# Optimization experiments

Hardware: AMD Instinct MI355X
Metric: run time of the kernel (lower is better)

Reference implementation:

```python
import jax, jax.numpy as jnp
import numpy as np

B, N, DIM, H = 32, 3136, 768, 12
C = DIM // H  # head_dim = 64


def setup_inputs() -> dict:
    key = jax.random.key(0)
    k1, k2, k3, k4 = jax.random.split(key, 4)
    x = jax.random.normal(k1, (B, N, DIM), dtype=jnp.float32)
    # Linear weights stored as (in, out); qkv has no bias (qkv_bias=False)
    w_qkv = jax.random.normal(k2, (DIM, 3 * DIM), dtype=jnp.float32) * (1.0 / np.sqrt(DIM))
    w_proj = jax.random.normal(k3, (DIM, DIM), dtype=jnp.float32) * (1.0 / np.sqrt(DIM))
    b_proj = jax.random.normal(k4, (DIM,), dtype=jnp.float32) * 0.01
    return {"x": x, "w_qkv": w_qkv, "w_proj": w_proj, "b_proj": b_proj}


def reference(x, w_qkv, w_proj, b_proj):
    # qkv projection: [B,N,3*DIM] -> [3,B,H,N,C]
    qkv = (x @ w_qkv).reshape(B, N, 3, H, C).transpose(2, 0, 3, 1, 4)
    q, k, v = qkv[0], qkv[1], qkv[2]
    # Efficient (linear) attention: softmax q over channel dim, k over token dim
    q = jax.nn.softmax(q, axis=-1)                      # [B,H,N,C], softmax over C
    kt = jax.nn.softmax(k.transpose(0, 1, 3, 2), axis=-1)  # [B,H,C,N], softmax over N
    context = jnp.einsum('bhcn,bhnd->bhcd', kt, v)      # [B,H,C,C]
    out = jnp.einsum('bhnc,bhcd->bhnd', q, context)     # [B,H,N,C]
    out = out.transpose(0, 2, 1, 3).reshape(B, N, DIM)  # [B,N,DIM]
    return out @ w_proj + b_proj
```

## Files before the change

kernel.cpp:

```cpp
#include <hip/hip_runtime.h>
#include <hip/hip_bf16.h>

typedef __attribute__((ext_vector_type(8))) short bf16x8;
typedef __attribute__((ext_vector_type(4))) float f32x4;

constexpr int BATCH = 32, SEQ = 3136, DIM = 768, NH = 12, HD = 64;
constexpr int M_TOT = BATCH * SEQ;
constexpr int QKVC  = 3 * DIM;
constexpr int GK    = 768;
constexpr int NKT   = GK / 64;

__device__ __forceinline__ float bf2f(unsigned short u) {
  union { unsigned int i; float f; } x; x.i = ((unsigned int)u) << 16; return x.f;
}
__device__ __forceinline__ unsigned short f2bf(float f) {
  union { float f; unsigned int i; } x; x.f = f;
  unsigned int r = x.i + 0x7FFFu + ((x.i >> 16) & 1u);
  return (unsigned short)(r >> 16);
}
__device__ __forceinline__ unsigned int pack2(float lo, float hi) {
  return (unsigned int)f2bf(lo) | ((unsigned int)f2bf(hi) << 16);
}
__device__ __forceinline__ void gload_lds16(const unsigned short* g, unsigned short* l) {
  __builtin_amdgcn_global_load_lds(
      (const __attribute__((address_space(1))) void*)g,
      (__attribute__((address_space(3))) void*)l, 16, 0, 0);
}

#define BARX()  asm volatile("s_barrier" ::: "memory")
#define LGKM0() asm volatile("s_waitcnt lgkmcnt(0)" ::: "memory")
#define VM8()   asm volatile("s_waitcnt vmcnt(8)" ::: "memory")
#define VM4()   asm volatile("s_waitcnt vmcnt(4)" ::: "memory")
#define VM0()   asm volatile("s_waitcnt vmcnt(0)" ::: "memory")
#define SB0()   __builtin_amdgcn_sched_barrier(0)

__global__ void conv_kernel(const float* __restrict__ in, unsigned short* __restrict__ out, long n) {
  long i = ((long)blockIdx.x * blockDim.x + threadIdx.x) * 8;
  long stride = (long)gridDim.x * blockDim.x * 8;
  for (; i < n; i += stride) {
    float4 a = *(const float4*)(in + i);
    float4 b = *(const float4*)(in + i + 4);
    uint4 o;
    o.x = pack2(a.x, a.y); o.y = pack2(a.z, a.w);
    o.z = pack2(b.x, b.y); o.w = pack2(b.z, b.w);
    *(uint4*)(out + i) = o;
  }
}

__global__ void transp_kernel(const float* __restrict__ w, unsigned short* __restrict__ wt, int K, int N) {
  __shared__ float tile[32][33];
  int n0 = blockIdx.x * 32, k0 = blockIdx.y * 32;
  int tx = threadIdx.x, ty = threadIdx.y;
  #pragma unroll
  for (int i = 0; i < 32; i += 8)
    tile[ty + i][tx] = w[(size_t)(k0 + ty + i) * N + n0 + tx];
  __syncthreads();
  #pragma unroll
  for (int i = 0; i < 32; i += 8)
    wt[(size_t)(n0 + ty + i) * K + k0 + tx] = f2bf(tile[tx][ty + i]);
}

__device__ __forceinline__ void stage_half(const unsigned short* __restrict__ G, long row0, int col0,
                                           unsigned short* ldsHalf, int t) {
  int r = t >> 2;
  int gslot = (t & 3) ^ ((t >> 3) & 3);
  char* dst = (char*)ldsHalf + ((t >> 6) << 10);
  gload_lds16(G + (row0 + r) * (long)GK + col0 + gslot * 8, (unsigned short*)dst);
  gload_lds16(G + (row0 + 128 + r) * (long)GK + col0 + gslot * 8, (unsigned short*)(dst + 8192));
}
__device__ __forceinline__ bf16x8 frag(const unsigned short* half, int r, int ko) {
  return *(const bf16x8*)((const char*)half + r * 64 + ((((ko >> 3) ^ ((r >> 1) & 3))) << 4));
}

#define MM16(Q) do { \
  acc[(Q)*4+0][0]=__builtin_amdgcn_mfma_f32_16x16x32_bf16(a0,b0,acc[(Q)*4+0][0],0,0,0); \
  acc[(Q)*4+0][1]=__builtin_amdgcn_mfma_f32_16x16x32_bf16(a0,b1,acc[(Q)*4+0][1],0,0,0); \
  acc[(Q)*4+0][2]=__builtin_amdgcn_mfma_f32_16x16x32_bf16(a0,b2,acc[(Q)*4+0][2],0,0,0); \
  acc[(Q)*4+0][3]=__builtin_amdgcn_mfma_f32_16x16x32_bf16(a0,b3,acc[(Q)*4+0][3],0,0,0); \
  acc[(Q)*4+1][0]=__builtin_amdgcn_mfma_f32_16x16x32_bf16(a1,b0,acc[(Q)*4+1][0],0,0,0); \
  acc[(Q)*4+1][1]=__builtin_amdgcn_mfma_f32_16x16x32_bf16(a1,b1,acc[(Q)*4+1][1],0,0,0); \
  acc[(Q)*4+1][2]=__builtin_amdgcn_mfma_f32_16x16x32_bf16(a1,b2,acc[(Q)*4+1][2],0,0,0); \
  acc[(Q)*4+1][3]=__builtin_amdgcn_mfma_f32_16x16x32_bf16(a1,b3,acc[(Q)*4+1][3],0,0,0); \
  acc[(Q)*4+2][0]=__builtin_amdgcn_mfma_f32_16x16x32_bf16(a2,b0,acc[(Q)*4+2][0],0,0,0); \
  acc[(Q)*4+2][1]=__builtin_amdgcn_mfma_f32_16x16x32_bf16(a2,b1,acc[(Q)*4+2][1],0,0,0); \
  acc[(Q)*4+2][2]=__builtin_amdgcn_mfma_f32_16x16x32_bf16(a2,b2,acc[(Q)*4+2][2],0,0,0); \
  acc[(Q)*4+2][3]=__builtin_amdgcn_mfma_f32_16x16x32_bf16(a2,b3,acc[(Q)*4+2][3],0,0,0); \
  acc[(Q)*4+3][0]=__builtin_amdgcn_mfma_f32_16x16x32_bf16(a3,b0,acc[(Q)*4+3][0],0,0,0); \
  acc[(Q)*4+3][1]=__builtin_amdgcn_mfma_f32_16x16x32_bf16(a3,b1,acc[(Q)*4+3][1],0,0,0); \
  acc[(Q)*4+3][2]=__builtin_amdgcn_mfma_f32_16x16x32_bf16(a3,b2,acc[(Q)*4+3][2],0,0,0); \
  acc[(Q)*4+3][3]=__builtin_amdgcn_mfma_f32_16x16x32_bf16(a3,b3,acc[(Q)*4+3][3],0,0,0); \
} while (0)

#define KTILE(J, BUF, N2, N3) { \
  const unsigned short* Ah0 = &lds[BUF][0][0][0]; \
  const unsigned short* Bh0 = &lds[BUF][1][0][0]; \
  const unsigned short* Ah1 = &lds[BUF][0][1][0]; \
  const unsigned short* Bh1 = &lds[BUF][1][1][0]; \
  bf16x8 a0, a1, a2, a3, b0, b1, b2, b3; \
   \
  a0 = frag(Ah0, ra,      ko); a1 = frag(Ah0, ra + 16, ko); \
  a2 = frag(Ah0, ra + 32, ko); a3 = frag(Ah0, ra + 48, ko); \
  b0 = frag(Bh0, rb,      ko); b1 = frag(Bh0, rb + 16, ko); \
  b2 = frag(Bh0, rb + 32, ko); b3 = frag(Bh0, rb + 48, ko); \
  if (N2) stage_half(A, m0, ((J) + 1) * 64 + 32, &lds[(BUF) ^ 1][0][1][0], t); \
  BARX(); LGKM0(); SB0(); \
  __builtin_amdgcn_s_setprio(1); MM16(0); __builtin_amdgcn_s_setprio(0); BARX(); \
   \
  a0 = frag(Ah0, ra + 64, ko); a1 = frag(Ah0, ra + 80, ko); \
  a2 = frag(Ah0, ra + 96, ko); a3 = frag(Ah0, ra + 112, ko); \
  if (N2) stage_half(Bt, n0, ((J) + 1) * 64 + 32, &lds[(BUF) ^ 1][1][1][0], t); \
  if (N2) { VM8(); } else { VM0(); } \
  BARX(); LGKM0(); SB0(); \
  __builtin_amdgcn_s_setprio(1); MM16(1); __builtin_amdgcn_s_setprio(0); BARX(); \
   \
  a0 = frag(Ah1, ra,      ko); a1 = frag(Ah1, ra + 16, ko); \
  a2 = frag(Ah1, ra + 32, ko); a3 = frag(Ah1, ra + 48, ko); \
  b0 = frag(Bh1, rb,      ko); b1 = frag(Bh1, rb + 16, ko); \
  b2 = frag(Bh1, rb + 32, ko); b3 = frag(Bh1, rb + 48, ko); \
  if (N3) stage_half(A, m0, ((J) + 2) * 64, &lds[BUF][0][0][0], t); \
  BARX(); LGKM0(); SB0(); \
  __builtin_amdgcn_s_setprio(1); MM16(0); __builtin_amdgcn_s_setprio(0); BARX(); \
   \
  a0 = frag(Ah1, ra + 64, ko); a1 = frag(Ah1, ra + 80, ko); \
  a2 = frag(Ah1, ra + 96, ko); a3 = frag(Ah1, ra + 112, ko); \
  if (N3) stage_half(Bt, n0, ((J) + 2) * 64, &lds[BUF][1][0][0], t); \
  if (N2) { if (N3) { VM8(); } else { VM4(); } } \
  BARX(); LGKM0(); SB0(); \
  __builtin_amdgcn_s_setprio(1); MM16(1); __builtin_amdgcn_s_setprio(0); BARX(); \
}

template<int OUTMODE>
__global__ __launch_bounds__(512, 2) void gemm256(const unsigned short* __restrict__ A,
                                                  const unsigned short* __restrict__ Bt,
                                                  void* __restrict__ Cp,
                                                  const float* __restrict__ bias,
                                                  int Nld, int MT) {
  __shared__ unsigned short lds[2][2][2][8192];
  int t = threadIdx.x, lane = t & 63, wid = t >> 6;
  int wm = wid >> 2, wn = wid & 3;
  int cpx = (int)gridDim.x >> 3;
  int wg = ((int)blockIdx.x & 7) * cpx + ((int)blockIdx.x >> 3);
  int mt = wg % MT, nt = wg / MT;
  long m0 = (long)mt * 256, n0 = (long)nt * 256;
  int fl = lane & 15, ko = (lane >> 4) * 8;
  int ra = wm * 128 + fl, rb = wn * 64 + fl;
  f32x4 acc[8][4] = {};
  stage_half(A,  m0, 0,  &lds[0][0][0][0], t);
  stage_half(Bt, n0, 0,  &lds[0][1][0][0], t);
  stage_half(A,  m0, 32, &lds[0][0][1][0], t);
  stage_half(Bt, n0, 32, &lds[0][1][1][0], t);
  stage_half(A,  m0, 64, &lds[1][0][0][0], t);
  stage_half(Bt, n0, 64, &lds[1][1][0][0], t);
  VM8(); BARX();
  #pragma unroll 1
  for (int jp = 0; jp < 5; ++jp) {
    int j0 = jp * 2;
    KTILE(j0,     0, true, true);
    KTILE(j0 + 1, 1, true, true);
  }
  KTILE(10, 0, true,  false);
  KTILE(11, 1, false, false);
  int r0 = (lane >> 4) * 4;
  #pragma unroll
  for (int mf = 0; mf < 8; ++mf) {
    #pragma unroll
    for (int nf = 0; nf < 4; ++nf) {
      long row = m0 + wm * 128 + mf * 16 + r0;
      int col = (int)n0 + wn * 64 + nf * 16 + fl;
      if (OUTMODE == 0) {
        unsigned short* C = (unsigned short*)Cp;
        bool doexp = (n0 < 2 * DIM);
        #pragma unroll
        for (int r = 0; r < 4; ++r) {
          float v = acc[mf][nf][r];
          C[(size_t)(row + r) * Nld + col] = f2bf(doexp ? __expf(v) : v);
        }
      } else {
        float* C = (float*)Cp;
        float bb = bias[col];
        #pragma unroll
        for (int r = 0; r < 4; ++r)
          C[(size_t)(row + r) * Nld + col] = acc[mf][nf][r] + bb;
      }
    }
  }
}

__global__ void ctx_kernel(const unsigned short* __restrict__ qkv, unsigned short* __restrict__ ctxT) {
  int bh = blockIdx.x;
  int b = bh / NH, h = bh % NH;
  __shared__ unsigned short Et[64 * 40];
  __shared__ unsigned short Vt[64 * 40];
  __shared__ float denom[64];
  int t = threadIdx.x, lane = t & 63, w = t >> 6;
  if (t < 64) denom[t] = 0.0f;
  int nl = t >> 3, e0 = (t & 7) * 8;
  int ko = (lane >> 4) * 8, fl = lane & 15;
  size_t base = (size_t)b * SEQ * QKVC + (size_t)h * HD;
  float dp[8] = {};
  f32x4 acc[4] = {};
  for (int c0 = 0; c0 < SEQ; c0 += 32) {
    __syncthreads();
    size_t rb = base + (size_t)(c0 + nl) * QKVC;
    uint4 kvec = *(const uint4*)(qkv + rb + DIM + e0);
    uint4 vvec = *(const uint4*)(qkv + rb + 2 * DIM + e0);
    const unsigned short* kp = (const unsigned short*)&kvec;
    const unsigned short* vp = (const unsigned short*)&vvec;
    #pragma unroll
    for (int j = 0; j < 8; ++j) {
      dp[j] += bf2f(kp[j]);
      Et[(e0 + j) * 40 + nl] = kp[j];
      Vt[(e0 + j) * 40 + nl] = vp[j];
    }
    __syncthreads();
    bf16x8 af = *(const bf16x8*)(Et + (w * 16 + fl) * 40 + ko);
    #pragma unroll
    for (int nf = 0; nf < 4; ++nf) {
      bf16x8 bv = *(const bf16x8*)(Vt + (nf * 16 + fl) * 40 + ko);
      acc[nf] = __builtin_amdgcn_mfma_f32_16x16x32_bf16(af, bv, acc[nf], 0, 0, 0);
    }
  }
  #pragma unroll
  for (int j = 0; j < 8; ++j) atomicAdd(&denom[e0 + j], dp[j]);
  __syncthreads();
  int r0 = (lane >> 4) * 4;
  unsigned short* outp = ctxT + (size_t)bh * 4096;
  #pragma unroll
  for (int nf = 0; nf < 4; ++nf)
    #pragma unroll
    for (int r = 0; r < 4; ++r) {
      int c = w * 16 + r0 + r;
      int d = nf * 16 + fl;
      outp[d * 64 + c] = f2bf(acc[nf][r] / denom[c]);
    }
}

__global__ void pv_kernel(const unsigned short* __restrict__ qkv, const unsigned short* __restrict__ ctxT,
                          unsigned short* __restrict__ aout) {
  int bid = blockIdx.x;
  int bh = bid / 49, chunk = bid - bh * 49;
  int b = bh / NH, h = bh % NH;
  int n0 = chunk * 64;
  __shared__ unsigned short P[64 * 80];
  __shared__ unsigned short CT[64 * 80];
  __shared__ float srow[64];
  int t = threadIdx.x, lane = t & 63, w = t >> 6;
  int ko = (lane >> 4) * 8, fl = lane & 15;
  if (t < 64) srow[t] = 0.0f;
  {
    int d = t >> 2, cq = (t & 3) * 16;
    const uint4* src = (const uint4*)(ctxT + (size_t)bh * 4096 + d * 64 + cq);
    *(uint4*)(CT + d * 80 + cq) = src[0];
    *(uint4*)(CT + d * 80 + cq + 8) = src[1];
  }
  __syncthreads();
  {
    int nl = t >> 2, cq = (t & 3) * 16;
    size_t rb = (size_t)(b * SEQ + n0 + nl) * QKVC + h * HD + cq;
    uint4 q0 = *(const uint4*)(qkv + rb);
    uint4 q1 = *(const uint4*)(qkv + rb + 8);
    *(uint4*)(P + nl * 80 + cq) = q0;
    *(uint4*)(P + nl * 80 + cq + 8) = q1;
    const unsigned short* qp0 = (const unsigned short*)&q0;
    const unsigned short* qp1 = (const unsigned short*)&q1;
    float s = 0.0f;
    #pragma unroll
    for (int j = 0; j < 8; ++j) s += bf2f(qp0[j]) + bf2f(qp1[j]);
    atomicAdd(&srow[nl], s);
  }
  __syncthreads();
  f32x4 acc[4] = {};
  #pragma unroll
  for (int kk = 0; kk < 2; ++kk) {
    bf16x8 af = *(const bf16x8*)(P + (w * 16 + fl) * 80 + kk * 32 + ko);
    #pragma unroll
    for (int nf = 0; nf < 4; ++nf) {
      bf16x8 bv = *(const bf16x8*)(CT + (nf * 16 + fl) * 80 + kk * 32 + ko);
      acc[nf] = __builtin_amdgcn_mfma_f32_16x16x32_bf16(af, bv, acc[nf], 0, 0, 0);
    }
  }
  int r0 = (lane >> 4) * 4;
  #pragma unroll
  for (int nf = 0; nf < 4; ++nf)
    #pragma unroll
    for (int r = 0; r < 4; ++r) {
      int nlr = w * 16 + r0 + r;
      int d = nf * 16 + fl;
      float v = acc[nf][r] / srow[nlr];
      aout[(size_t)(b * SEQ + n0 + nlr) * DIM + h * HD + d] = f2bf(v);
    }
}

extern "C" void kernel_launch(void* const* d_in, const int* in_sizes, int n_in,
                              void* d_out, int out_size, void* d_ws, size_t ws_size,
                              hipStream_t stream) {
  const float* x      = (const float*)d_in[0];
  const float* w_qkv  = (const float*)d_in[1];
  const float* w_proj = (const float*)d_in[2];
  const float* b_proj = (const float*)d_in[3];
  char* ws = (char*)d_ws;
  unsigned short* x_bf    = (unsigned short*)(ws);
  unsigned short* wt_qkv  = (unsigned short*)(ws + 154140672);
  unsigned short* wt_proj = (unsigned short*)(ws + 157679616);
  unsigned short* qkv     = (unsigned short*)(ws + 158859264);
  unsigned short* ctxT    = (unsigned short*)(ws + 154140672);
  unsigned short* aout    = (unsigned short*)(ws);

  conv_kernel<<<2048, 256, 0, stream>>>(x, x_bf, (long)M_TOT * DIM);
  transp_kernel<<<dim3(QKVC / 32, DIM / 32), dim3(32, 8), 0, stream>>>(w_qkv, wt_qkv, DIM, QKVC);
  transp_kernel<<<dim3(DIM / 32, DIM / 32), dim3(32, 8), 0, stream>>>(w_proj, wt_proj, DIM, DIM);
  gemm256<0><<<(M_TOT / 256) * (QKVC / 256), 512, 0, stream>>>(x_bf, wt_qkv, qkv, nullptr,
                                                               QKVC, M_TOT / 256);
  ctx_kernel<<<BATCH * NH, 256, 0, stream>>>(qkv, ctxT);
  pv_kernel<<<BATCH * NH * (SEQ / 64), 256, 0, stream>>>(qkv, ctxT, aout);
  gemm256<1><<<(M_TOT / 256) * (DIM / 256), 512, 0, stream>>>(aout, wt_proj, (float*)d_out, b_proj,
                                                              DIM, M_TOT / 256);
}
```

Baseline: 867.1 us.

## Make GEMMs persistent with cross-tile prefetch and split context reduction

```diff
diff --git a/kernel.cpp b/kernel.cpp
--- a/kernel.cpp
+++ b/kernel.cpp
@@ -8,7 +8,6 @@
 constexpr int M_TOT = BATCH * SEQ;
 constexpr int QKVC  = 3 * DIM;
 constexpr int GK    = 768;
-constexpr int NKT   = GK / 64;
 
 __device__ __forceinline__ float bf2f(unsigned short u) {
   union { unsigned int i; float f; } x; x.i = ((unsigned int)u) << 16; return x.f;
@@ -30,8 +29,6 @@
 #define BARX()  asm volatile("s_barrier" ::: "memory")
 #define LGKM0() asm volatile("s_waitcnt lgkmcnt(0)" ::: "memory")
 #define VM8()   asm volatile("s_waitcnt vmcnt(8)" ::: "memory")
-#define VM4()   asm volatile("s_waitcnt vmcnt(4)" ::: "memory")
-#define VM0()   asm volatile("s_waitcnt vmcnt(0)" ::: "memory")
 #define SB0()   __builtin_amdgcn_sched_barrier(0)
 
 __global__ void conv_kernel(const float* __restrict__ in, unsigned short* __restrict__ out, long n) {
@@ -91,7 +88,7 @@
   acc[(Q)*4+3][3]=__builtin_amdgcn_mfma_f32_16x16x32_bf16(a3,b3,acc[(Q)*4+3][3],0,0,0); \
 } while (0)
 
-#define KTILE(J, BUF, N2, N3) { \
+#define KTILE_U(BUF, MA2, NB2, C2, MA3, NB3, C3) { \
   const unsigned short* Ah0 = &lds[BUF][0][0][0]; \
   const unsigned short* Bh0 = &lds[BUF][1][0][0]; \
   const unsigned short* Ah1 = &lds[BUF][0][1][0]; \
@@ -102,14 +99,14 @@
   a2 = frag(Ah0, ra + 32, ko); a3 = frag(Ah0, ra + 48, ko); \
   b0 = frag(Bh0, rb,      ko); b1 = frag(Bh0, rb + 16, ko); \
   b2 = frag(Bh0, rb + 32, ko); b3 = frag(Bh0, rb + 48, ko); \
-  if (N2) stage_half(A, m0, ((J) + 1) * 64 + 32, &lds[(BUF) ^ 1][0][1][0], t); \
+  stage_half(A, MA2, C2, &lds[(BUF) ^ 1][0][1][0], t); \
   BARX(); LGKM0(); SB0(); \
   __builtin_amdgcn_s_setprio(1); MM16(0); __builtin_amdgcn_s_setprio(0); BARX(); \
    \
   a0 = frag(Ah0, ra + 64, ko); a1 = frag(Ah0, ra + 80, ko); \
   a2 = frag(Ah0, ra + 96, ko); a3 = frag(Ah0, ra + 112, ko); \
-  if (N2) stage_half(Bt, n0, ((J) + 1) * 64 + 32, &lds[(BUF) ^ 1][1][1][0], t); \
-  if (N2) { VM8(); } else { VM0(); } \
+  stage_half(Bt, NB2, C2, &lds[(BUF) ^ 1][1][1][0], t); \
+  VM8(); \
   BARX(); LGKM0(); SB0(); \
   __builtin_amdgcn_s_setprio(1); MM16(1); __builtin_amdgcn_s_setprio(0); BARX(); \
    \
@@ -117,77 +114,91 @@
   a2 = frag(Ah1, ra + 32, ko); a3 = frag(Ah1, ra + 48, ko); \
   b0 = frag(Bh1, rb,      ko); b1 = frag(Bh1, rb + 16, ko); \
   b2 = frag(Bh1, rb + 32, ko); b3 = frag(Bh1, rb + 48, ko); \
-  if (N3) stage_half(A, m0, ((J) + 2) * 64, &lds[BUF][0][0][0], t); \
+  stage_half(A, MA3, C3, &lds[BUF][0][0][0], t); \
   BARX(); LGKM0(); SB0(); \
   __builtin_amdgcn_s_setprio(1); MM16(0); __builtin_amdgcn_s_setprio(0); BARX(); \
    \
   a0 = frag(Ah1, ra + 64, ko); a1 = frag(Ah1, ra + 80, ko); \
   a2 = frag(Ah1, ra + 96, ko); a3 = frag(Ah1, ra + 112, ko); \
-  if (N3) stage_half(Bt, n0, ((J) + 2) * 64, &lds[BUF][1][0][0], t); \
-  if (N2) { if (N3) { VM8(); } else { VM4(); } } \
+  stage_half(Bt, NB3, C3, &lds[BUF][1][0][0], t); \
+  VM8(); \
   BARX(); LGKM0(); SB0(); \
   __builtin_amdgcn_s_setprio(1); MM16(1); __builtin_amdgcn_s_setprio(0); BARX(); \
 }
 
-template<int OUTMODE>
-__global__ __launch_bounds__(512, 2) void gemm256(const unsigned short* __restrict__ A,
-                                                  const unsigned short* __restrict__ Bt,
-                                                  void* __restrict__ Cp,
-                                                  const float* __restrict__ bias,
-                                                  int Nld, int MT) {
+template<int OUTMODE, int NT>
+__global__ __launch_bounds__(512, 2) void gemm256p(const unsigned short* __restrict__ A,
+                                                   const unsigned short* __restrict__ Bt,
+                                                   void* __restrict__ Cp,
+                                                   const float* __restrict__ bias,
+                                                   int Nld, int TPX) {
   __shared__ unsigned short lds[2][2][2][8192];
   int t = threadIdx.x, lane = t & 63, wid = t >> 6;
   int wm = wid >> 2, wn = wid & 3;
-  int cpx = (int)gridDim.x >> 3;
-  int wg = ((int)blockIdx.x & 7) * cpx + ((int)blockIdx.x >> 3);
-  int mt = wg % MT, nt = wg / MT;
-  long m0 = (long)mt * 256, n0 = (long)nt * 256;
+  int bid = (int)blockIdx.x;
+  int xcd = bid & 7, slot = bid >> 3;
+  int tau = xcd * TPX + slot;
+  int tend = (xcd + 1) * TPX;
   int fl = lane & 15, ko = (lane >> 4) * 8;
   int ra = wm * 128 + fl, rb = wn * 64 + fl;
-  f32x4 acc[8][4] = {};
-  stage_half(A,  m0, 0,  &lds[0][0][0][0], t);
-  stage_half(Bt, n0, 0,  &lds[0][1][0][0], t);
-  stage_half(A,  m0, 32, &lds[0][0][1][0], t);
-  stage_half(Bt, n0, 32, &lds[0][1][1][0], t);
-  stage_half(A,  m0, 64, &lds[1][0][0][0], t);
-  stage_half(Bt, n0, 64, &lds[1][1][0][0], t);
-  VM8(); BARX();
+  f32x4 acc[8][4];
+  {
+    long m0 = (long)(tau / NT) * 256, n0 = (long)(tau % NT) * 256;
+    stage_half(A,  m0, 0,  &lds[0][0][0][0], t);
+    stage_half(Bt, n0, 0,  &lds[0][1][0][0], t);
+    stage_half(A,  m0, 32, &lds[0][0][1][0], t);
+    stage_half(Bt, n0, 32, &lds[0][1][1][0], t);
+    stage_half(A,  m0, 64, &lds[1][0][0][0], t);
+    stage_half(Bt, n0, 64, &lds[1][1][0][0], t);
+    VM8(); BARX();
+  }
   #pragma unroll 1
-  for (int jp = 0; jp < 5; ++jp) {
-    int j0 = jp * 2;
-    KTILE(j0,     0, true, true);
-    KTILE(j0 + 1, 1, true, true);
-  }
-  KTILE(10, 0, true,  false);
-  KTILE(11, 1, false, false);
-  int r0 = (lane >> 4) * 4;
-  #pragma unroll
-  for (int mf = 0; mf < 8; ++mf) {
-    #pragma unroll
-    for (int nf = 0; nf < 4; ++nf) {
-      long row = m0 + wm * 128 + mf * 16 + r0;
-      int col = (int)n0 + wn * 64 + nf * 16 + fl;
-      if (OUTMODE == 0) {
-        unsigned short* C = (unsigned short*)Cp;
-        bool doexp = (n0 < 2 * DIM);
-        #pragma unroll
-        for (int r = 0; r < 4; ++r) {
-          float v = acc[mf][nf][r];
-          C[(size_t)(row + r) * Nld + col] = f2bf(doexp ? __expf(v) : v);
+  for (; tau < tend; tau += 32) {
+    long m0 = (long)(tau / NT) * 256, n0 = (long)(tau % NT) * 256;
+    int tn = (tau + 32 < tend) ? tau + 32 : tau;
+    long m0n = (long)(tn / NT) * 256, n0n = (long)(tn % NT) * 256;
+    #pragma unroll
+    for (int i = 0; i < 8; ++i)
+      #pragma unroll
+      for (int j2 = 0; j2 < 4; ++j2) acc[i][j2] = (f32x4){0.f, 0.f, 0.f, 0.f};
+    #pragma unroll 1
+    for (int j = 0; j < 10; j += 2) {
+      KTILE_U(0, m0, n0, j * 64 + 96,  m0, n0, j * 64 + 128);
+      KTILE_U(1, m0, n0, j * 64 + 160, m0, n0, j * 64 + 192);
+    }
+    KTILE_U(0, m0,  n0,  736, m0n, n0n, 0);
+    KTILE_U(1, m0n, n0n, 32,  m0n, n0n, 64);
+    int r0 = (lane >> 4) * 4;
+    #pragma unroll
+    for (int mf = 0; mf < 8; ++mf) {
+      #pragma unroll
+      for (int nf = 0; nf < 4; ++nf) {
+        long row = m0 + wm * 128 + mf * 16 + r0;
+        int col = (int)n0 + wn * 64 + nf * 16 + fl;
+        if (OUTMODE == 0) {
+          unsigned short* C = (unsigned short*)Cp;
+          bool doexp = (n0 < 2 * DIM);
+          #pragma unroll
+          for (int r = 0; r < 4; ++r) {
+            float v = acc[mf][nf][r];
+            C[(size_t)(row + r) * Nld + col] = f2bf(doexp ? __expf(v) : v);
+          }
+        } else {
+          float* C = (float*)Cp;
+          float bb = bias[col];
+          #pragma unroll
+          for (int r = 0; r < 4; ++r)
+            C[(size_t)(row + r) * Nld + col] = acc[mf][nf][r] + bb;
         }
-      } else {
-        float* C = (float*)Cp;
-        float bb = bias[col];
-        #pragma unroll
-        for (int r = 0; r < 4; ++r)
-          C[(size_t)(row + r) * Nld + col] = acc[mf][nf][r] + bb;
       }
     }
   }
 }
 
-__global__ void ctx_kernel(const unsigned short* __restrict__ qkv, unsigned short* __restrict__ ctxT) {
-  int bh = blockIdx.x;
+__global__ void ctx_part(const unsigned short* __restrict__ qkv, float* __restrict__ part,
+                         float* __restrict__ dpart) {
+  int blk = blockIdx.x;
+  int bh = blk / 7, ch = blk - bh * 7;
   int b = bh / NH, h = bh % NH;
   __shared__ unsigned short Et[64 * 40];
   __shared__ unsigned short Vt[64 * 40];
@@ -199,7 +210,8 @@
   size_t base = (size_t)b * SEQ * QKVC + (size_t)h * HD;
   float dp[8] = {};
   f32x4 acc[4] = {};
-  for (int c0 = 0; c0 < SEQ; c0 += 32) {
+  int c0b = ch * 448;
+  for (int c0 = c0b; c0 < c0b + 448; c0 += 32) {
     __syncthreads();
     size_t rb = base + (size_t)(c0 + nl) * QKVC;
     uint4 kvec = *(const uint4*)(qkv + rb + DIM + e0);
@@ -224,15 +236,34 @@
   for (int j = 0; j < 8; ++j) atomicAdd(&denom[e0 + j], dp[j]);
   __syncthreads();
   int r0 = (lane >> 4) * 4;
-  unsigned short* outp = ctxT + (size_t)bh * 4096;
+  float* pp = part + (size_t)blk * 4096;
   #pragma unroll
   for (int nf = 0; nf < 4; ++nf)
     #pragma unroll
     for (int r = 0; r < 4; ++r) {
       int c = w * 16 + r0 + r;
       int d = nf * 16 + fl;
-      outp[d * 64 + c] = f2bf(acc[nf][r] / denom[c]);
-    }
+      pp[d * 64 + c] = acc[nf][r];
+    }
+  if (t < 64) dpart[blk * 64 + t] = denom[t];
+}
+
+__global__ void ctx_reduce(const float* __restrict__ part, const float* __restrict__ dpart,
+                           unsigned short* __restrict__ ctxT) {
+  int bh = blockIdx.x, t = threadIdx.x;
+  const float* pp = part + (size_t)bh * 7 * 4096;
+  const float* dd = dpart + (size_t)bh * 7 * 64;
+  #pragma unroll
+  for (int i = 0; i < 16; ++i) {
+    int idx = i * 256 + t;
+    float s = 0.f, ds = 0.f;
+    #pragma unroll
+    for (int c = 0; c < 7; ++c) {
+      s += pp[c * 4096 + idx];
+      ds += dd[c * 64 + (idx & 63)];
+    }
+    ctxT[(size_t)bh * 4096 + idx] = f2bf(s / ds);
+  }
 }
 
 __global__ void pv_kernel(const unsigned short* __restrict__ qkv, const unsigned short* __restrict__ ctxT,
@@ -304,15 +335,16 @@
   unsigned short* wt_proj = (unsigned short*)(ws + 157679616);
   unsigned short* qkv     = (unsigned short*)(ws + 158859264);
   unsigned short* ctxT    = (unsigned short*)(ws + 154140672);
-  unsigned short* aout    = (unsigned short*)(ws);
+  float* part  = (float*)(ws);
+  float* dpart = (float*)(ws + 44040192);
+  unsigned short* aout = (unsigned short*)(ws);
 
   conv_kernel<<<2048, 256, 0, stream>>>(x, x_bf, (long)M_TOT * DIM);
   transp_kernel<<<dim3(QKVC / 32, DIM / 32), dim3(32, 8), 0, stream>>>(w_qkv, wt_qkv, DIM, QKVC);
   transp_kernel<<<dim3(DIM / 32, DIM / 32), dim3(32, 8), 0, stream>>>(w_proj, wt_proj, DIM, DIM);
-  gemm256<0><<<(M_TOT / 256) * (QKVC / 256), 512, 0, stream>>>(x_bf, wt_qkv, qkv, nullptr,
-                                                               QKVC, M_TOT / 256);
-  ctx_kernel<<<BATCH * NH, 256, 0, stream>>>(qkv, ctxT);
+  gemm256p<0, 9><<<256, 512, 0, stream>>>(x_bf, wt_qkv, qkv, nullptr, QKVC, 441);
+  ctx_part<<<BATCH * NH * 7, 256, 0, stream>>>(qkv, part, dpart);
+  ctx_reduce<<<BATCH * NH, 256, 0, stream>>>(part, dpart, ctxT);
   pv_kernel<<<BATCH * NH * (SEQ / 64), 256, 0, stream>>>(qkv, ctxT, aout);
-  gemm256<1><<<(M_TOT / 256) * (DIM / 256), 512, 0, stream>>>(aout, wt_proj, (float*)d_out, b_proj,
-                                                              DIM, M_TOT / 256);
-}
+  gemm256p<1, 3><<<256, 512, 0, stream>>>(aout, wt_proj, (float*)d_out, b_proj, DIM, 147);
+}
```

Result: faster. 810.7 us (-6.5%).
